# Optimization experiments

Hardware: AMD Instinct MI355X
Metric: run time of the kernel (lower is better)

Reference implementation:

```python
import jax, jax.numpy as jnp
import numpy as np

L, H, D, F = 6, 8, 512, 2048
B, T, S = 8, 512, 1024
DK = D // H


def setup_inputs() -> dict:
    key = jax.random.key(0)
    ks = jax.random.split(key, 16)
    p = lambda k, shape: jax.random.normal(k, shape, jnp.float32) * 0.02
    inp = {
        "tgt": jax.random.normal(ks[0], (B, T, D), jnp.float32),
        "memory": jax.random.normal(ks[1], (B, S, D), jnp.float32),
        "source_mask": jnp.ones((B, 1, 1, S), jnp.int32),
        "target_mask": jnp.broadcast_to(jnp.tril(jnp.ones((T, T), jnp.int32)), (B, 1, T, T)),
        # self-attention params, stacked over layers
        "sa_wq": p(ks[2], (L, D, D)), "sa_wk": p(ks[3], (L, D, D)),
        "sa_wv": p(ks[4], (L, D, D)), "sa_wo": p(ks[5], (L, D, D)),
        "sa_bq": jnp.zeros((L, D)), "sa_bk": jnp.zeros((L, D)),
        "sa_bv": jnp.zeros((L, D)), "sa_bo": jnp.zeros((L, D)),
        # cross-attention params
        "ca_wq": p(ks[6], (L, D, D)), "ca_wk": p(ks[7], (L, D, D)),
        "ca_wv": p(ks[8], (L, D, D)), "ca_wo": p(ks[9], (L, D, D)),
        "ca_bq": jnp.zeros((L, D)), "ca_bk": jnp.zeros((L, D)),
        "ca_bv": jnp.zeros((L, D)), "ca_bo": jnp.zeros((L, D)),
        # FFN params
        "ff_w1": p(ks[10], (L, D, F)), "ff_b1": jnp.zeros((L, F)),
        "ff_w2": p(ks[11], (L, F, D)), "ff_b2": jnp.zeros((L, D)),
        # single shared LayerNorm (as in the original module)
        "ln_g": jnp.ones((D,)), "ln_b": jnp.zeros((D,)),
    }
    return inp


def _layernorm(x, g, b, eps=1e-5):
    m = jnp.mean(x, axis=-1, keepdims=True)
    v = jnp.var(x, axis=-1, keepdims=True)
    return (x - m) * jax.lax.rsqrt(v + eps) * g + b


def _mha(xq, xk, xv, wq, bq, wk, bk, wv, bv, wo, bo, mask):
    Bq = xq.shape[0]
    proj = lambda x, w, b: (x @ w + b).reshape(Bq, -1, H, DK).transpose(0, 2, 1, 3)
    q, k, v = proj(xq, wq, bq), proj(xk, wk, bk), proj(xv, wv, bv)  # [B,H,*,DK]
    scores = jnp.einsum('bhtd,bhsd->bhts', q, k) / jnp.sqrt(jnp.float32(DK))
    scores = jnp.where(mask == 0, jnp.float32(-1e9), scores)
    p_attn = jax.nn.softmax(scores, axis=-1)
    o = jnp.einsum('bhts,bhsd->bhtd', p_attn, v)
    o = o.transpose(0, 2, 1, 3).reshape(Bq, -1, H * DK)
    return o @ wo + bo


def reference(tgt, memory, source_mask, target_mask,
              sa_wq, sa_wk, sa_wv, sa_wo, sa_bq, sa_bk, sa_bv, sa_bo,
              ca_wq, ca_wk, ca_wv, ca_wo, ca_bq, ca_bk, ca_bv, ca_bo,
              ff_w1, ff_b1, ff_w2, ff_b2, ln_g, ln_b):
    output = tgt
    for i in range(L):
        # NOTE: faithful to original code: self-attn block uses `tgt`, not `output`
        n = _layernorm(tgt, ln_g, ln_b)
        output = tgt + _mha(n, n, n,
                            sa_wq[i], sa_bq[i], sa_wk[i], sa_bk[i],
                            sa_wv[i], sa_bv[i], sa_wo[i], sa_bo[i], target_mask)
        n = _layernorm(output, ln_g, ln_b)
        output = output + _mha(n, memory, memory,
                               ca_wq[i], ca_bq[i], ca_wk[i], ca_bk[i],
                               ca_wv[i], ca_bv[i], ca_wo[i], ca_bo[i], source_mask)
        n = _layernorm(output, ln_g, ln_b)
        ff = jax.nn.relu(n @ ff_w1[i] + ff_b1[i]) @ ff_w2[i] + ff_b2[i]
        output = output + ff
    return _layernorm(output, ln_g, ln_b)
```

## Files before the change

kernel.cpp:

```cpp
#include <hip/hip_runtime.h>

typedef __bf16 bf16;
typedef unsigned short u16;
typedef __bf16 bf16x8 __attribute__((ext_vector_type(8)));
typedef float f32x4 __attribute__((ext_vector_type(4)));

#define GLL16(gp, lp)                                                        \
    __builtin_amdgcn_global_load_lds(                                        \
        (const __attribute__((address_space(1))) void*)(gp),                 \
        (__attribute__((address_space(3))) void*)(lp), 16, 0, 0)

__device__ __forceinline__ bool is_f32(const void* lng_raw) {
    return ((const unsigned int*)lng_raw)[0] == 0x3F800000u;
}

__device__ __forceinline__ float ldf(const void* base, size_t idx, bool f32) {
    return f32 ? ((const float*)base)[idx] : (float)((const bf16*)base)[idx];
}

__device__ __forceinline__ uint4 load8(const void* base, size_t idx, bool f) {
    if (!f) return *(const uint4*)((const bf16*)base + idx);
    const float* p = (const float*)base + idx;
    float4 a = ((const float4*)p)[0], b = ((const float4*)p)[1];
    union { uint4 u; bf16 h[8]; } r;
    r.h[0] = (bf16)a.x; r.h[1] = (bf16)a.y; r.h[2] = (bf16)a.z; r.h[3] = (bf16)a.w;
    r.h[4] = (bf16)b.x; r.h[5] = (bf16)b.y; r.h[6] = (bf16)b.z; r.h[7] = (bf16)b.w;
    return r.u;
}

__global__ void pack_vecs_k(const void* sbq, const void* sbk, const void* sbv,
                            const void* sbo, const void* cbq, const void* cbk,
                            const void* cbv, const void* cbo, const void* fb1,
                            const void* fb2, const void* lng, const void* lnb,
                            bf16* __restrict__ dst) {
    int i = blockIdx.x * 256 + threadIdx.x;
    bool f = is_f32(lng);
    const int L5D = 5 * 512, L5F = 5 * 2048;
    float v;
    if (i < 512) v = ldf(sbq, L5D + i, f);
    else if (i < 1024) v = ldf(sbk, L5D + i - 512, f);
    else if (i < 1536) v = ldf(sbv, L5D + i - 1024, f);
    else if (i < 2048) v = ldf(cbk, L5D + i - 1536, f);
    else if (i < 2560) v = ldf(cbv, L5D + i - 2048, f);
    else if (i < 3072) v = ldf(sbo, L5D + i - 2560, f);
    else if (i < 3584) v = ldf(cbq, L5D + i - 3072, f);
    else if (i < 4096) v = ldf(cbo, L5D + i - 3584, f);
    else if (i < 6144) v = ldf(fb1, L5F + i - 4096, f);
    else if (i < 6656) v = ldf(fb2, L5D + i - 6144, f);
    else if (i < 7168) v = ldf(lng, i - 6656, f);
    else v = ldf(lnb, i - 7168, f);
    dst[i] = (bf16)v;
}

struct SrcList { const void* p[10]; };
struct DstList { u16* p[10]; };
__global__ __launch_bounds__(256) void prep_w_k(SrcList SL, DstList DL,
                                                const void* __restrict__ lng) {
    __shared__ u16 tile[32][33];
    bool f = is_f32(lng);
    int t = blockIdx.x;
    int widx, R, C, tile_id;
    if (t < 2048) { widx = t >> 8; R = 512; C = 512; tile_id = t & 255; }
    else if (t < 3072) { widx = 8; R = 512; C = 2048; tile_id = t - 2048; }
    else { widx = 9; R = 2048; C = 512; tile_id = t - 3072; }
    int tpr = C >> 5;
    int cx = (tile_id % tpr) * 32, ry = (tile_id / tpr) * 32;
    size_t off = (widx < 8) ? (size_t)5 * 512 * 512 : (size_t)5 * 512 * 2048;
    const void* src = SL.p[widx];
    u16* dst = DL.p[widx];
    int tx = threadIdx.x & 31, ty = threadIdx.x >> 5;
#pragma unroll
    for (int i = 0; i < 32; i += 8) {
        bf16 bv = (bf16)ldf(src, off + (size_t)(ry + ty + i) * C + cx + tx, f);
        tile[ty + i][tx] = *(u16*)&bv;
    }
    __syncthreads();
#pragma unroll
    for (int i = 0; i < 32; i += 8)
        dst[(size_t)(cx + ty + i) * R + ry + tx] = tile[tx][ty + i];
}

__global__ __launch_bounds__(256) void vt2_k(const bf16* __restrict__ qkv,
                                             const bf16* __restrict__ kvca,
                                             bf16* __restrict__ vt_sa,
                                             bf16* __restrict__ vt_ca) {
    __shared__ u16 tile[32][33];
    int bid = blockIdx.x;
    const u16* src;
    u16* dst;
    int S, ld, coff, xs, ys, bh;
    if (bid < 2048) {
        src = (const u16*)qkv; dst = (u16*)vt_sa; S = 512; ld = 1536; coff = 1024;
        xs = bid & 15; ys = (bid >> 4) & 1; bh = bid >> 5;
    } else {
        int t = bid - 2048;
        src = (const u16*)kvca; dst = (u16*)vt_ca; S = 1024; ld = 1024; coff = 512;
        xs = t & 31; ys = (t >> 5) & 1; bh = t >> 6;
    }
    int b = bh >> 3, h = bh & 7;
    int s0 = xs * 32, d0 = ys * 32;
    int tx = threadIdx.x & 31, ty = threadIdx.x >> 5;
#pragma unroll
    for (int i = 0; i < 32; i += 8)
        tile[ty + i][tx] = src[(size_t)(b * S + s0 + ty + i) * ld + coff + h * 64 + d0 + tx];
    __syncthreads();
#pragma unroll
    for (int i = 0; i < 32; i += 8)
        dst[((size_t)bh * 64 + d0 + ty + i) * S + s0 + tx] = tile[tx][ty + i];
}

template <typename TIN>
__global__ __launch_bounds__(256) void ln_kernel(const TIN* __restrict__ x,
                                                 bf16* __restrict__ out,
                                                 const bf16* __restrict__ g,
                                                 const bf16* __restrict__ bb) {
    int row = blockIdx.x * 4 + (threadIdx.x >> 6);
    int lane = threadIdx.x & 63;
    const TIN* xr = x + (size_t)row * 512 + lane * 8;
    float v[8];
    if constexpr (sizeof(TIN) == 2) {
        uint4 u = *(const uint4*)xr;
        const bf16* p = (const bf16*)&u;
#pragma unroll
        for (int i = 0; i < 8; ++i) v[i] = (float)p[i];
    } else {
        float4 a = ((const float4*)xr)[0];
        float4 b2 = ((const float4*)xr)[1];
        v[0] = a.x; v[1] = a.y; v[2] = a.z; v[3] = a.w;
        v[4] = b2.x; v[5] = b2.y; v[6] = b2.z; v[7] = b2.w;
    }
    float s = 0.f, s2 = 0.f;
#pragma unroll
    for (int i = 0; i < 8; ++i) { s += v[i]; s2 += v[i] * v[i]; }
#pragma unroll
    for (int off = 32; off >= 1; off >>= 1) {
        s += __shfl_xor(s, off);
        s2 += __shfl_xor(s2, off);
    }
    float mean = s * (1.f / 512.f);
    float var = fmaxf(s2 * (1.f / 512.f) - mean * mean, 0.f);
    float rstd = rsqrtf(var + 1e-5f);
    int col = lane * 8;
    __align__(16) bf16 o8[8];
#pragma unroll
    for (int i = 0; i < 8; ++i)
        o8[i] = (bf16)((v[i] - mean) * rstd * (float)g[col + i] + (float)bb[col + i]);
    *(uint4*)(out + (size_t)row * 512 + col) = *(const uint4*)o8;
}

__global__ __launch_bounds__(256) void ln_any_k(const void* __restrict__ x,
                                                bf16* __restrict__ out,
                                                const bf16* __restrict__ g,
                                                const bf16* __restrict__ bb) {
    bool f = is_f32(g - 512);
    (void)f;
}

__global__ __launch_bounds__(256) void ln_raw_k(const void* __restrict__ x,
                                                bf16* __restrict__ out,
                                                const bf16* __restrict__ g,
                                                const bf16* __restrict__ bb,
                                                const void* __restrict__ lng_raw) {
    bool f = is_f32(lng_raw);
    int row = blockIdx.x * 4 + (threadIdx.x >> 6);
    int lane = threadIdx.x & 63;
    size_t base = (size_t)row * 512 + lane * 8;
    float v[8];
    if (f) {
        const float* xr = (const float*)x + base;
        float4 a = ((const float4*)xr)[0], b2 = ((const float4*)xr)[1];
        v[0] = a.x; v[1] = a.y; v[2] = a.z; v[3] = a.w;
        v[4] = b2.x; v[5] = b2.y; v[6] = b2.z; v[7] = b2.w;
    } else {
        uint4 u = *(const uint4*)((const bf16*)x + base);
        const bf16* p = (const bf16*)&u;
#pragma unroll
        for (int i = 0; i < 8; ++i) v[i] = (float)p[i];
    }
    float s = 0.f, s2 = 0.f;
#pragma unroll
    for (int i = 0; i < 8; ++i) { s += v[i]; s2 += v[i] * v[i]; }
#pragma unroll
    for (int off = 32; off >= 1; off >>= 1) {
        s += __shfl_xor(s, off);
        s2 += __shfl_xor(s2, off);
    }
    float mean = s * (1.f / 512.f);
    float var = fmaxf(s2 * (1.f / 512.f) - mean * mean, 0.f);
    float rstd = rsqrtf(var + 1e-5f);
    int col = lane * 8;
    __align__(16) bf16 o8[8];
#pragma unroll
    for (int i = 0; i < 8; ++i)
        o8[i] = (bf16)((v[i] - mean) * rstd * (float)g[col + i] + (float)bb[col + i]);
    *(uint4*)(out + (size_t)row * 512 + col) = *(const uint4*)o8;
}

__global__ __launch_bounds__(256) void ln_final_k(const float* __restrict__ x,
                                                  void* __restrict__ out,
                                                  const bf16* __restrict__ g,
                                                  const bf16* __restrict__ bb,
                                                  const void* __restrict__ lng_raw) {
    int row = blockIdx.x * 4 + (threadIdx.x >> 6);
    int lane = threadIdx.x & 63;
    const float* xr = x + (size_t)row * 512 + lane * 8;
    float v[8];
    float4 a = ((const float4*)xr)[0];
    float4 b2 = ((const float4*)xr)[1];
    v[0] = a.x; v[1] = a.y; v[2] = a.z; v[3] = a.w;
    v[4] = b2.x; v[5] = b2.y; v[6] = b2.z; v[7] = b2.w;
    float s = 0.f, s2 = 0.f;
#pragma unroll
    for (int i = 0; i < 8; ++i) { s += v[i]; s2 += v[i] * v[i]; }
#pragma unroll
    for (int off = 32; off >= 1; off >>= 1) {
        s += __shfl_xor(s, off);
        s2 += __shfl_xor(s2, off);
    }
    float mean = s * (1.f / 512.f);
    float var = fmaxf(s2 * (1.f / 512.f) - mean * mean, 0.f);
    float rstd = rsqrtf(var + 1e-5f);
    int col = lane * 8;
    float o[8];
#pragma unroll
    for (int i = 0; i < 8; ++i)
        o[i] = (v[i] - mean) * rstd * (float)g[col + i] + (float)bb[col + i];
    if (is_f32(lng_raw)) {
        float* op = (float*)out + (size_t)row * 512 + col;
        ((float4*)op)[0] = make_float4(o[0], o[1], o[2], o[3]);
        ((float4*)op)[1] = make_float4(o[4], o[5], o[6], o[7]);
    } else {
        __align__(16) bf16 o8[8];
#pragma unroll
        for (int i = 0; i < 8; ++i) o8[i] = (bf16)o[i];
        *(uint4*)((bf16*)out + (size_t)row * 512 + col) = *(const uint4*)o8;
    }
}

template <int TM, int ASRC, int RES, bool RELU, int DB, typename OUT_T>
__device__ __forceinline__ void gemm_body(const void* A, const bf16* Bt, const bf16* bias,
                                          const void* res, OUT_T* C,
                                          int K, int lda, int ldc,
                                          int m0, int n0, bool f, bf16* lA, bf16* lB) {
    constexpr int MI = TM / 32;
    constexpr int AR = TM / 64;
    int tid = threadIdx.x;
    int w = tid >> 6, lane = tid & 63, quad = lane >> 4, c = lane & 15;
    int wm = (w >> 1) * (TM / 2), wn = (w & 1) * 64;
    f32x4 acc[MI][4] = {};
    uint4 ald[AR];

    auto issueB = [&](int kt, int bs) {
        bf16* sB = lB + bs * (128 * 32);
#pragma unroll
        for (int r = 0; r < 2; ++r) {
            int id = r * 256 + tid;
            int rw = id >> 2, ch = id & 3;
            GLL16(&Bt[(size_t)(n0 + rw) * K + kt + ch * 8], &sB[id * 8]);
        }
    };
    auto issueA = [&](int kt, int bs) {
        bf16* sA = lA + bs * (TM * 32);
#pragma unroll
        for (int r = 0; r < AR; ++r) {
            int id = r * 256 + tid;
            int rw = id >> 2, ch = id & 3;
            if (ASRC == 0) {
                GLL16(&((const bf16*)A)[(size_t)(m0 + rw) * lda + kt + ch * 8], &sA[id * 8]);
            } else {
                ald[r] = load8(A, (size_t)(m0 + rw) * lda + kt + ch * 8, f);
            }
        }
    };
    auto writeA = [&](int bs) {
        if (ASRC == 0) return;
        bf16* sA = lA + bs * (TM * 32);
#pragma unroll
        for (int r = 0; r < AR; ++r) {
            int id = r * 256 + tid;
            *(uint4*)&sA[id * 8] = ald[r];
        }
    };
    auto compute = [&](int bs) {
        bf16* sA = lA + bs * (TM * 32);
        bf16* sB = lB + bs * (128 * 32);
        bf16x8 af[MI], bfr[4];
#pragma unroll
        for (int i = 0; i < MI; ++i) af[i] = *(const bf16x8*)&sA[(wm + i * 16 + c) * 32 + quad * 8];
#pragma unroll
        for (int i = 0; i < 4; ++i) bfr[i] = *(const bf16x8*)&sB[(wn + i * 16 + c) * 32 + quad * 8];
#pragma unroll
        for (int mi = 0; mi < MI; ++mi)
#pragma unroll
            for (int ni = 0; ni < 4; ++ni)
                acc[mi][ni] = __builtin_amdgcn_mfma_f32_16x16x32_bf16(
                    af[mi], bfr[ni], acc[mi][ni], 0, 0, 0);
    };

    if (DB == 0) {
        for (int kt = 0; kt < K; kt += 32) {
            __syncthreads();
            issueA(kt, 0);
            writeA(0);
            issueB(kt, 0);
            __syncthreads();
            compute(0);
        }
    } else {
        issueB(0, 0);
        issueA(0, 0);
        writeA(0);
        __syncthreads();
        int cur = 0;
        for (int kt = 0; kt < K; kt += 32) {
            bool more = (kt + 32 < K);
            if (more) { issueB(kt + 32, cur ^ 1); issueA(kt + 32, cur ^ 1); }
            compute(cur);
            if (more) writeA(cur ^ 1);
            __syncthreads();
            cur ^= 1;
        }
    }

    bool fR = (RES == 1) ? f : false;
#pragma unroll
    for (int mi = 0; mi < MI; ++mi) {
#pragma unroll
        for (int ni = 0; ni < 4; ++ni) {
#pragma unroll
            for (int r = 0; r < 4; ++r) {
                int row = m0 + wm + mi * 16 + quad * 4 + r;
                int col = n0 + wn + ni * 16 + c;
                float v = acc[mi][ni][r] + (float)bias[col];
                if (RELU) v = fmaxf(v, 0.f);
                if (RES == 1) v += ldf(res, (size_t)row * 512 + col, fR);
                if (RES == 2) v += ((const float*)res)[(size_t)row * 512 + col];
                C[(size_t)row * ldc + col] = (OUT_T)v;
            }
        }
    }
}

__global__ __launch_bounds__(256) void gemm_qkv_cakv(const bf16* __restrict__ nbuf,
                                                     const void* __restrict__ mem,
                                                     const bf16* __restrict__ wqkv,
                                                     const bf16* __restrict__ wcakv,
                                                     const bf16* __restrict__ cvec,
                                                     bf16* __restrict__ qkv,
                                                     bf16* __restrict__ kvca,
                                                     const void* __restrict__ lng_raw) {
    __shared__ __align__(16) bf16 lA[128 * 32];
    __shared__ __align__(16) bf16 lB[128 * 32];
    int bid = blockIdx.x;
    if (bid < 384) {
        gemm_body<128, 0, 0, false, 0, bf16>(nbuf, wqkv, cvec, nullptr, qkv, 512, 512, 1536,
                                             (bid & 31) * 128, (bid >> 5) * 128, false, lA, lB);
    } else {
        int t = bid - 384;
        gemm_body<128, 1, 0, false, 0, bf16>(mem, wcakv, cvec + 1536, nullptr, kvca, 512, 512, 1024,
                                             (t & 63) * 128, (t >> 6) * 128, is_f32(lng_raw), lA, lB);
    }
}

template <int TM, int RES, bool RELU, int DB, typename OUT_T>
__global__ __launch_bounds__(256) void gemmN(const void* __restrict__ A,
                                             const bf16* __restrict__ Bt,
                                             const bf16* __restrict__ bias,
                                             const void* __restrict__ res,
                                             OUT_T* __restrict__ C,
                                             int K, int lda, int ldc,
                                             const void* __restrict__ lng_raw) {
    __shared__ __align__(16) bf16 lA[(DB + 1) * TM * 32];
    __shared__ __align__(16) bf16 lB[(DB + 1) * 128 * 32];
    bool f = (RES == 1) ? is_f32(lng_raw) : false;
    gemm_body<TM, 0, RES, RELU, DB, OUT_T>(A, Bt, bias, res, C, K, lda, ldc,
                                           blockIdx.x * TM, blockIdx.y * 128, f, lA, lB);
}

template <bool CAUSAL>
__global__ __launch_bounds__(256) void attn2_k(const bf16* __restrict__ Qb, int ldq,
                                               const bf16* __restrict__ Kb, int ldk,
                                               const bf16* __restrict__ Vt,
                                               const int* __restrict__ smask,
                                               bf16* __restrict__ O, int ldo,
                                               int Tq, int Skv) {
    __shared__ __align__(16) bf16 QPs[64 * 64];
    __shared__ __align__(16) bf16 Ks[64 * 64];
    __shared__ __align__(16) bf16 Vts[64 * 64];
    int tid = threadIdx.x;
    int bh = blockIdx.x, qt = blockIdx.y;
    int b = bh >> 3, h = bh & 7;
    int qbase = qt * 64, hoff = h * 64;
    int w = tid >> 6, lane = tid & 63, quad = lane >> 4, c = lane & 15;

#pragma unroll
    for (int r = 0; r < 2; ++r) {
        int id = r * 256 + tid;
        int rw = id >> 3, ch = id & 7;
        *(uint4*)&QPs[rw * 64 + ((ch ^ (rw & 7)) << 3)] =
            *(const uint4*)&Qb[(size_t)(b * Tq + qbase + rw) * ldq + hoff + ch * 8];
    }
    __syncthreads();
    bf16x8 qf[2];
    {
        int row = w * 16 + c;
        qf[0] = *(const bf16x8*)&QPs[row * 64 + ((quad ^ (row & 7)) << 3)];
        qf[1] = *(const bf16x8*)&QPs[row * 64 + (((4 + quad) ^ (row & 7)) << 3)];
    }

    float m_st[4] = {-1e4f, -1e4f, -1e4f, -1e4f};
    float l_st[4] = {0.f, 0.f, 0.f, 0.f};
    f32x4 o_acc[4] = {};
    bf16* Pw = QPs + w * 1024;

    int nkb = CAUSAL ? (qt + 1) : (Skv >> 6);
    uint4 kr[2], vr[2];
    auto issue = [&](int j) {
        int kbase = j * 64;
#pragma unroll
        for (int r = 0; r < 2; ++r) {
            int id = r * 256 + tid;
            int rw = id >> 3, ch = id & 7;
            kr[r] = *(const uint4*)&Kb[(size_t)(b * Skv + kbase + rw) * ldk + hoff + ch * 8];
            vr[r] = *(const uint4*)&Vt[((size_t)bh * 64 + rw) * Skv + kbase + ch * 8];
        }
    };
    issue(0);

    for (int j = 0; j < nkb; ++j) {
        int kbase = j * 64;
        __syncthreads();
#pragma unroll
        for (int r = 0; r < 2; ++r) {
            int id = r * 256 + tid;
            int rw = id >> 3, ch = id & 7;
            int sw = (ch ^ (rw & 7)) << 3;
            *(uint4*)&Ks[rw * 64 + sw] = kr[r];
            *(uint4*)&Vts[rw * 64 + sw] = vr[r];
        }
        __syncthreads();
        if (j + 1 < nkb) issue(j + 1);

        f32x4 sv[4] = {};
#pragma unroll
        for (int ni = 0; ni < 4; ++ni) {
            int row = ni * 16 + c;
#pragma unroll
            for (int kk = 0; kk < 2; ++kk) {
                bf16x8 kf = *(const bf16x8*)&Ks[row * 64 + ((((kk << 2) + quad) ^ (row & 7)) << 3)];
                sv[ni] = __builtin_amdgcn_mfma_f32_16x16x32_bf16(qf[kk], kf, sv[ni], 0, 0, 0);
            }
        }
        int kg[4];
        bool okm[4];
#pragma unroll
        for (int ni = 0; ni < 4; ++ni) {
            kg[ni] = kbase + ni * 16 + c;
            okm[ni] = CAUSAL ? true : (smask[b * Skv + kg[ni]] != 0);
        }
#pragma unroll
        for (int r = 0; r < 4; ++r) {
            int q_row = quad * 4 + r;
            int qg = qbase + w * 16 + q_row;
            float vv[4];
            float rm = -1e4f;
#pragma unroll
            for (int ni = 0; ni < 4; ++ni) {
                bool ok = CAUSAL ? (kg[ni] <= qg) : okm[ni];
                vv[ni] = ok ? sv[ni][r] * 0.125f : -1e4f;
                rm = fmaxf(rm, vv[ni]);
            }
#pragma unroll
            for (int off = 1; off < 16; off <<= 1) rm = fmaxf(rm, __shfl_xor(rm, off));
            float mn = fmaxf(m_st[r], rm);
            float alpha = __expf(m_st[r] - mn);
            float rs = 0.f;
#pragma unroll
            for (int ni = 0; ni < 4; ++ni) {
                bool ok = CAUSAL ? (kg[ni] <= qg) : okm[ni];
                float p = ok ? __expf(vv[ni] - mn) : 0.f;
                rs += p;
                int col = ni * 16 + c;
                Pw[q_row * 64 + ((((col >> 3) ^ (q_row & 7)) << 3) | (col & 7))] = (bf16)p;
            }
#pragma unroll
            for (int off = 1; off < 16; off <<= 1) rs += __shfl_xor(rs, off);
            l_st[r] = l_st[r] * alpha + rs;
            m_st[r] = mn;
#pragma unroll
            for (int dt = 0; dt < 4; ++dt) o_acc[dt][r] *= alpha;
        }
        bf16x8 pf[2];
        pf[0] = *(const bf16x8*)&Pw[c * 64 + ((quad ^ (c & 7)) << 3)];
        pf[1] = *(const bf16x8*)&Pw[c * 64 + (((4 + quad) ^ (c & 7)) << 3)];
#pragma unroll
        for (int dt = 0; dt < 4; ++dt) {
            int row = dt * 16 + c;
#pragma unroll
            for (int kk = 0; kk < 2; ++kk) {
                bf16x8 vf = *(const bf16x8*)&Vts[row * 64 + ((((kk << 2) + quad) ^ (row & 7)) << 3)];
                o_acc[dt] = __builtin_amdgcn_mfma_f32_16x16x32_bf16(pf[kk], vf, o_acc[dt], 0, 0, 0);
            }
        }
    }

#pragma unroll
    for (int r = 0; r < 4; ++r) {
        float inv = 1.f / fmaxf(l_st[r], 1e-20f);
        int orow = b * Tq + qbase + w * 16 + quad * 4 + r;
#pragma unroll
        for (int dt = 0; dt < 4; ++dt)
            O[(size_t)orow * ldo + hoff + dt * 16 + c] = (bf16)(o_acc[dt][r] * inv);
    }
}

extern "C" void kernel_launch(void* const* d_in, const int* in_sizes, int n_in,
                              void* d_out, int out_size, void* d_ws, size_t ws_size,
                              hipStream_t stream) {
    (void)in_sizes; (void)n_in; (void)out_size; (void)ws_size;
    const size_t DD = (size_t)512 * 512;
    const int* smask = (const int*)d_in[2];
    const void* lng_raw = d_in[24];

    char* ws = (char*)d_ws;
    size_t off = 0;
    auto alloc = [&](size_t bytes) { void* p = ws + off; off += (bytes + 255) & ~(size_t)255; return p; };
    bf16* wt_qkv = (bf16*)alloc(1536 * 512 * 2);
    bf16* wt_sao = (bf16*)alloc(512 * 512 * 2);
    bf16* wt_caq = (bf16*)alloc(512 * 512 * 2);
    bf16* wt_cakv = (bf16*)alloc(1024 * 512 * 2);
    bf16* wt_cao = (bf16*)alloc(512 * 512 * 2);
    bf16* wt_ff1 = (bf16*)alloc(2048 * 512 * 2);
    bf16* wt_ff2 = (bf16*)alloc(512 * 2048 * 2);
    bf16* cvec = (bf16*)alloc(7680 * 2);
    bf16* nbuf = (bf16*)alloc((size_t)4096 * 512 * 2);
    bf16* attn = (bf16*)alloc((size_t)4096 * 512 * 2);
    bf16* qca = (bf16*)alloc((size_t)4096 * 512 * 2);
    float* x = (float*)alloc((size_t)4096 * 512 * 4);
    bf16* vt_sa = (bf16*)alloc((size_t)64 * 64 * 512 * 2);
    bf16* vt_ca = (bf16*)alloc((size_t)64 * 64 * 1024 * 2);
    bf16* kvca = (bf16*)alloc((size_t)8192 * 1024 * 2);
    bf16* big = (bf16*)alloc((size_t)4096 * 2048 * 2);
    bf16* qkv = big;
    bf16* hbuf = big;

    SrcList SL; DstList DL;
    SL.p[0] = d_in[4];  DL.p[0] = (u16*)wt_qkv;
    SL.p[1] = d_in[5];  DL.p[1] = (u16*)(wt_qkv + DD);
    SL.p[2] = d_in[6];  DL.p[2] = (u16*)(wt_qkv + 2 * DD);
    SL.p[3] = d_in[7];  DL.p[3] = (u16*)wt_sao;
    SL.p[4] = d_in[12]; DL.p[4] = (u16*)wt_caq;
    SL.p[5] = d_in[13]; DL.p[5] = (u16*)wt_cakv;
    SL.p[6] = d_in[14]; DL.p[6] = (u16*)(wt_cakv + DD);
    SL.p[7] = d_in[15]; DL.p[7] = (u16*)wt_cao;
    SL.p[8] = d_in[20]; DL.p[8] = (u16*)wt_ff1;
    SL.p[9] = d_in[22]; DL.p[9] = (u16*)wt_ff2;
    prep_w_k<<<4096, 256, 0, stream>>>(SL, DL, lng_raw);
    pack_vecs_k<<<30, 256, 0, stream>>>(d_in[8], d_in[9], d_in[10], d_in[11],
                                        d_in[16], d_in[17], d_in[18], d_in[19],
                                        d_in[21], d_in[23], d_in[24], d_in[25],
                                        cvec);
    const bf16* lng = cvec + 6656;
    const bf16* lnb = cvec + 7168;

    ln_raw_k<<<1024, 256, 0, stream>>>(d_in[0], nbuf, lng, lnb, lng_raw);
    gemm_qkv_cakv<<<896, 256, 0, stream>>>(nbuf, d_in[1], wt_qkv, wt_cakv, cvec,
                                           qkv, kvca, lng_raw);
    vt2_k<<<6144, 256, 0, stream>>>(qkv, kvca, vt_sa, vt_ca);

    attn2_k<true><<<dim3(64, 8), 256, 0, stream>>>(
        qkv, 1536, qkv + 512, 1536, vt_sa, nullptr, attn, 512, 512, 512);
    gemmN<64, 1, false, 1, float><<<dim3(64, 4), 256, 0, stream>>>(
        attn, wt_sao, cvec + 2560, d_in[0], x, 512, 512, 512, lng_raw);

    ln_kernel<float><<<1024, 256, 0, stream>>>(x, nbuf, lng, lnb);
    gemmN<64, 0, false, 1, bf16><<<dim3(64, 4), 256, 0, stream>>>(
        nbuf, wt_caq, cvec + 3072, nullptr, qca, 512, 512, 512, lng_raw);
    attn2_k<false><<<dim3(64, 8), 256, 0, stream>>>(
        qca, 512, kvca, 1024, vt_ca, smask, attn, 512, 512, 1024);
    gemmN<64, 2, false, 1, float><<<dim3(64, 4), 256, 0, stream>>>(
        attn, wt_cao, cvec + 3584, x, x, 512, 512, 512, lng_raw);

    ln_kernel<float><<<1024, 256, 0, stream>>>(x, nbuf, lng, lnb);
    gemmN<128, 0, true, 1, bf16><<<dim3(32, 16), 256, 0, stream>>>(
        nbuf, wt_ff1, cvec + 4096, nullptr, hbuf, 512, 512, 2048, lng_raw);
    gemmN<64, 2, false, 1, float><<<dim3(64, 4), 256, 0, stream>>>(
        hbuf, wt_ff2, cvec + 6144, x, x, 2048, 2048, 512, lng_raw);

    ln_final_k<<<1024, 256, 0, stream>>>(x, d_out, lng, lnb, lng_raw);
}
```

Measured before the change: 405.4 us.

## Transpose attention MFMA operands so each lane owns one query row

Swaps the A/B operands of both MFMAs in the attention kernel so the score and output accumulators are transposed and each lane holds one query row. Softmax state becomes a scalar per lane, row reductions drop to two cross-quad shuffles, P is written to LDS as 4-element vectors, source-mask reads become int4 loads, and output stores become 8-byte vectors. It also removes the register prefetch of the next K/V tile and loads K/V straight into LDS inside the loop, which gives up global-load latency hiding. A dead stub kernel is deleted.

```diff
diff --git a/kernel.cpp b/kernel.cpp
--- a/kernel.cpp
+++ b/kernel.cpp
@@ -3,6 +3,7 @@
 typedef __bf16 bf16;
 typedef unsigned short u16;
 typedef __bf16 bf16x8 __attribute__((ext_vector_type(8)));
+typedef __bf16 bf16x4 __attribute__((ext_vector_type(4)));
 typedef float f32x4 __attribute__((ext_vector_type(4)));
 
 #define GLL16(gp, lp)                                                        \
@@ -148,14 +149,6 @@
     *(uint4*)(out + (size_t)row * 512 + col) = *(const uint4*)o8;
 }
 
-__global__ __launch_bounds__(256) void ln_any_k(const void* __restrict__ x,
-                                                bf16* __restrict__ out,
-                                                const bf16* __restrict__ g,
-                                                const bf16* __restrict__ bb) {
-    bool f = is_f32(g - 512);
-    (void)f;
-}
-
 __global__ __launch_bounds__(256) void ln_raw_k(const void* __restrict__ x,
                                                 bf16* __restrict__ out,
                                                 const bf16* __restrict__ g,
@@ -408,24 +401,12 @@
         qf[1] = *(const bf16x8*)&QPs[row * 64 + (((4 + quad) ^ (row & 7)) << 3)];
     }
 
-    float m_st[4] = {-1e4f, -1e4f, -1e4f, -1e4f};
-    float l_st[4] = {0.f, 0.f, 0.f, 0.f};
+    float m_st = -1e4f, l_st = 0.f;
     f32x4 o_acc[4] = {};
-    bf16* Pw = QPs + w * 1024;
-
+    char* Pw = (char*)(QPs + w * 1024);
+
+    int qg = qbase + w * 16 + c;
     int nkb = CAUSAL ? (qt + 1) : (Skv >> 6);
-    uint4 kr[2], vr[2];
-    auto issue = [&](int j) {
-        int kbase = j * 64;
-#pragma unroll
-        for (int r = 0; r < 2; ++r) {
-            int id = r * 256 + tid;
-            int rw = id >> 3, ch = id & 7;
-            kr[r] = *(const uint4*)&Kb[(size_t)(b * Skv + kbase + rw) * ldk + hoff + ch * 8];
-            vr[r] = *(const uint4*)&Vt[((size_t)bh * 64 + rw) * Skv + kbase + ch * 8];
-        }
-    };
-    issue(0);
 
     for (int j = 0; j < nkb; ++j) {
         int kbase = j * 64;
@@ -435,11 +416,12 @@
             int id = r * 256 + tid;
             int rw = id >> 3, ch = id & 7;
             int sw = (ch ^ (rw & 7)) << 3;
-            *(uint4*)&Ks[rw * 64 + sw] = kr[r];
-            *(uint4*)&Vts[rw * 64 + sw] = vr[r];
+            *(uint4*)&Ks[rw * 64 + sw] =
+                *(const uint4*)&Kb[(size_t)(b * Skv + kbase + rw) * ldk + hoff + ch * 8];
+            *(uint4*)&Vts[rw * 64 + sw] =
+                *(const uint4*)&Vt[((size_t)bh * 64 + rw) * Skv + kbase + ch * 8];
         }
         __syncthreads();
-        if (j + 1 < nkb) issue(j + 1);
 
         f32x4 sv[4] = {};
 #pragma unroll
@@ -448,69 +430,80 @@
 #pragma unroll
             for (int kk = 0; kk < 2; ++kk) {
                 bf16x8 kf = *(const bf16x8*)&Ks[row * 64 + ((((kk << 2) + quad) ^ (row & 7)) << 3)];
-                sv[ni] = __builtin_amdgcn_mfma_f32_16x16x32_bf16(qf[kk], kf, sv[ni], 0, 0, 0);
+                sv[ni] = __builtin_amdgcn_mfma_f32_16x16x32_bf16(kf, qf[kk], sv[ni], 0, 0, 0);
             }
         }
-        int kg[4];
-        bool okm[4];
+
+        float vv[4][4];
+        float rm = -1e4f;
 #pragma unroll
         for (int ni = 0; ni < 4; ++ni) {
-            kg[ni] = kbase + ni * 16 + c;
-            okm[ni] = CAUSAL ? true : (smask[b * Skv + kg[ni]] != 0);
-        }
-#pragma unroll
-        for (int r = 0; r < 4; ++r) {
-            int q_row = quad * 4 + r;
-            int qg = qbase + w * 16 + q_row;
-            float vv[4];
-            float rm = -1e4f;
-#pragma unroll
-            for (int ni = 0; ni < 4; ++ni) {
-                bool ok = CAUSAL ? (kg[ni] <= qg) : okm[ni];
-                vv[ni] = ok ? sv[ni][r] * 0.125f : -1e4f;
-                rm = fmaxf(rm, vv[ni]);
+            int kv0 = kbase + ni * 16 + quad * 4;
+            if (CAUSAL) {
+#pragma unroll
+                for (int r = 0; r < 4; ++r) {
+                    vv[ni][r] = (kv0 + r <= qg) ? sv[ni][r] * 0.125f : -1e4f;
+                    rm = fmaxf(rm, vv[ni][r]);
+                }
+            } else {
+                int4 mk = *(const int4*)&smask[b * Skv + kv0];
+                const int* mp = (const int*)&mk;
+#pragma unroll
+                for (int r = 0; r < 4; ++r) {
+                    vv[ni][r] = mp[r] ? sv[ni][r] * 0.125f : -1e4f;
+                    rm = fmaxf(rm, vv[ni][r]);
+                }
             }
-#pragma unroll
-            for (int off = 1; off < 16; off <<= 1) rm = fmaxf(rm, __shfl_xor(rm, off));
-            float mn = fmaxf(m_st[r], rm);
-            float alpha = __expf(m_st[r] - mn);
-            float rs = 0.f;
-#pragma unroll
-            for (int ni = 0; ni < 4; ++ni) {
-                bool ok = CAUSAL ? (kg[ni] <= qg) : okm[ni];
-                float p = ok ? __expf(vv[ni] - mn) : 0.f;
+        }
+        rm = fmaxf(rm, __shfl_xor(rm, 16));
+        rm = fmaxf(rm, __shfl_xor(rm, 32));
+        float mn = fmaxf(m_st, rm);
+        float alpha = __expf(m_st - mn);
+        float rs = 0.f;
+#pragma unroll
+        for (int ni = 0; ni < 4; ++ni) {
+            __align__(8) bf16 p4[4];
+#pragma unroll
+            for (int r = 0; r < 4; ++r) {
+                float p = (vv[ni][r] > -9.9e3f) ? __expf(vv[ni][r] - mn) : 0.f;
                 rs += p;
-                int col = ni * 16 + c;
-                Pw[q_row * 64 + ((((col >> 3) ^ (q_row & 7)) << 3) | (col & 7))] = (bf16)p;
+                p4[r] = (bf16)p;
             }
-#pragma unroll
-            for (int off = 1; off < 16; off <<= 1) rs += __shfl_xor(rs, off);
-            l_st[r] = l_st[r] * alpha + rs;
-            m_st[r] = mn;
-#pragma unroll
-            for (int dt = 0; dt < 4; ++dt) o_acc[dt][r] *= alpha;
-        }
+            int g = ni * 2 + (quad >> 1);
+            *(bf16x4*)(Pw + c * 128 + ((g ^ (c & 7)) << 4) + (quad & 1) * 8) =
+                *(const bf16x4*)p4;
+        }
+        rs += __shfl_xor(rs, 16);
+        rs += __shfl_xor(rs, 32);
+        l_st = l_st * alpha + rs;
+        m_st = mn;
+#pragma unroll
+        for (int dt = 0; dt < 4; ++dt)
+#pragma unroll
+            for (int r = 0; r < 4; ++r) o_acc[dt][r] *= alpha;
+
         bf16x8 pf[2];
-        pf[0] = *(const bf16x8*)&Pw[c * 64 + ((quad ^ (c & 7)) << 3)];
-        pf[1] = *(const bf16x8*)&Pw[c * 64 + (((4 + quad) ^ (c & 7)) << 3)];
+        pf[0] = *(const bf16x8*)(Pw + c * 128 + ((quad ^ (c & 7)) << 4));
+        pf[1] = *(const bf16x8*)(Pw + c * 128 + (((4 + quad) ^ (c & 7)) << 4));
 #pragma unroll
         for (int dt = 0; dt < 4; ++dt) {
             int row = dt * 16 + c;
 #pragma unroll
             for (int kk = 0; kk < 2; ++kk) {
                 bf16x8 vf = *(const bf16x8*)&Vts[row * 64 + ((((kk << 2) + quad) ^ (row & 7)) << 3)];
-                o_acc[dt] = __builtin_amdgcn_mfma_f32_16x16x32_bf16(pf[kk], vf, o_acc[dt], 0, 0, 0);
+                o_acc[dt] = __builtin_amdgcn_mfma_f32_16x16x32_bf16(vf, pf[kk], o_acc[dt], 0, 0, 0);
             }
         }
     }
 
-#pragma unroll
-    for (int r = 0; r < 4; ++r) {
-        float inv = 1.f / fmaxf(l_st[r], 1e-20f);
-        int orow = b * Tq + qbase + w * 16 + quad * 4 + r;
-#pragma unroll
-        for (int dt = 0; dt < 4; ++dt)
-            O[(size_t)orow * ldo + hoff + dt * 16 + c] = (bf16)(o_acc[dt][r] * inv);
+    float inv = 1.f / fmaxf(l_st, 1e-20f);
+    size_t orow = (size_t)(b * Tq + qbase + w * 16 + c);
+#pragma unroll
+    for (int dt = 0; dt < 4; ++dt) {
+        __align__(8) bf16 o4[4];
+#pragma unroll
+        for (int r = 0; r < 4; ++r) o4[r] = (bf16)(o_acc[dt][r] * inv);
+        *(bf16x4*)&O[orow * ldo + hoff + dt * 16 + quad * 4] = *(const bf16x4*)o4;
     }
 }
 
```

Result: faster. 366.3 us (-9.6%).
